# Kernel tuning notes

Measured on AMD Instinct MI355X. Metric: run time of the kernel, lower is better.

## Reference

```python
import jax, jax.numpy as jnp
import numpy as np
import math

B, H, L = 8, 256, 4096
C = 1            # channels
D_STATE = 64
DD = D_STATE // 2  # d = 32
DT_MIN, DT_MAX = 1e-3, 1e-1


def setup_inputs() -> dict:
    key = jax.random.key(0)
    ks = jax.random.split(key, 6)
    u = jax.random.normal(ks[0], (B, H, L), dtype=jnp.float32)
    # analytic init matching the torch module
    h_scale = jnp.exp(jnp.arange(H, dtype=jnp.float32) / H * math.log(DT_MAX / DT_MIN))  # (H,)
    angles = jnp.arange(DD, dtype=jnp.float32) * jnp.float32(np.pi)                      # (DD,)
    theta = jnp.einsum('c,h,d->chd', jnp.ones((C,), jnp.float32), h_scale, angles)       # (C,H,DD)
    a = -jnp.broadcast_to(h_scale[None, :, None], (C, H, DD)).astype(jnp.float32)        # (C,H,DD)
    D = jax.random.normal(ks[1], (C, H), dtype=jnp.float32)
    b_p = jax.random.normal(ks[2], (C, H, DD), dtype=jnp.float32)
    c_p = jax.random.normal(ks[3], (C, H, DD), dtype=jnp.float32)
    x0 = jax.random.normal(ks[4], (C, H, DD), dtype=jnp.float32)
    return {"u": u, "theta": theta, "a": a, "D": D, "b_p": b_p, "c_p": c_p, "x0": x0}


def fft_conv(u, f):
    # u: (B,H,L), f: (C,H,L) -> (B,C,H,L) causal conv via zero-padded FFT
    l = u.shape[-1]
    n = 2 * l
    u_f = jnp.fft.rfft(u, n=n)          # (B,H,n//2+1)
    f_f = jnp.fft.rfft(f, n=n)          # (C,H,n//2+1)
    y_f = jnp.einsum('bhl,chl->bchl', u_f, f_f)
    return jnp.fft.irfft(y_f, n=n)[..., :l]


def reference(u, theta, a, D, b_p, c_p, x0):
    l = u.shape[-1]
    T = 1.0 / (l - 1)
    zk = T * jnp.arange(l, dtype=jnp.float32)            # (L,)
    zk4 = zk[None, None, :, None]                         # (1,1,L,1)
    ls = -jnp.abs(a) + 1j * theta                         # (C,H,DD) complex
    term_0 = (jnp.exp(ls * T) - 1.0) / ls                 # (C,H,DD)
    # base_term: (C,H,L,DD)
    base_term = (2.0 * term_0[:, :, None, :] * jnp.exp(ls[:, :, None, :] * zk4)).real
    q = b_p * c_p                                         # (C,H,DD)
    f = jnp.einsum('chd,chld->chl', q, base_term)         # (C,H,L)
    y = fft_conv(u, f)                                    # (B,C,H,L)
    y = y + jnp.einsum('bhl,ch->bchl', u, D)
    # initial-condition term
    cos_term = 2.0 * T * jnp.exp(-jnp.abs(a)[:, :, None, :] * zk4) * jnp.cos(theta[:, :, None, :] * zk4)
    init = jnp.einsum('chd,chld->chl', 2.0 * (c_p * x0), cos_term)  # (C,H,L)
    y = y + init[None]                                    # broadcast over batch
    b = y.shape[0]
    return y.reshape(b, -1, l)                            # (B, C*H, L)
```

## Files before the change

### kernel.cpp

```cpp
#include <hip/hip_runtime.h>

#define BB 8
#define HH 256
#define LL 4096
#define STR 72

#define WS_H  0
#define WS_P  (2u*1024*1024)
#define WS_R  (4u*1024*1024)
#define WS_C1 (6u*1024*1024)
#define WS_C2 (6u*1024*1024 + 128u*1024)

typedef __attribute__((ext_vector_type(8))) short short8;
typedef __attribute__((ext_vector_type(4))) float f32x4;

static __device__ inline unsigned short f2bf(float x) {
    union { float f; unsigned u; } v; v.f = x;
    unsigned r = v.u + 0x7fffu + ((v.u >> 16) & 1u);
    return (unsigned short)(r >> 16);
}
static __device__ inline float bf2f(unsigned short us) {
    union { unsigned u; float f; } v; v.u = ((unsigned)us) << 16; return v.f;
}

#define CMUL(or_, oi_, ar_, ai_, br_, bi_) do { \
    float _tr = fmaf((ar_), (br_), -(ai_) * (bi_)); \
    float _ti = fmaf((ar_), (bi_), (ai_) * (br_)); \
    (or_) = _tr; (oi_) = _ti; } while (0)

__global__ __launch_bounds__(256) void s4_pre_kernel(
    const float* __restrict__ theta, const float* __restrict__ a,
    const float* __restrict__ b_p,   const float* __restrict__ c_p,
    const float* __restrict__ x0,
    unsigned short* __restrict__ Hm, unsigned short* __restrict__ Pm,
    unsigned short* __restrict__ Rm, float4* __restrict__ C1,
    float* __restrict__ C2)
{
    const int tid = threadIdx.x;
    const int h   = blockIdx.x;
    const int d   = tid & 31;
    const int kb  = tid >> 5;
    const float T = 1.0f / (LL - 1);
    __shared__ float h_s[64];

    const float lr = a[h * 32 + d];
    const float li = theta[h * 32 + d];
    float sn, cS;
    sincosf(li * T, &sn, &cS);
    const float er = expf(lr * T);
    const float Rr = er * cS, Ri = er * sn;
    const float den = lr * lr + li * li;
    const float t0r = ((Rr - 1.f) * lr + Ri * li) / den;
    const float t0i = (Ri * lr - (Rr - 1.f) * li) / den;
    const float qq  = b_p[h * 32 + d] * c_p[h * 32 + d];
    const float wre = 2.f * qq * t0r, wim = 2.f * qq * t0i;
    const float vv  = 4.f * T * c_p[h * 32 + d] * x0[h * 32 + d];

    float r2r, r2i, r4r, r4i, r8r, r8i, r16r, r16i, r32r, r32i;
    CMUL(r2r, r2i, Rr, Ri, Rr, Ri);
    CMUL(r4r, r4i, r2r, r2i, r2r, r2i);
    CMUL(r8r, r8i, r4r, r4i, r4r, r4i);
    CMUL(r16r, r16i, r8r, r8i, r8r, r8i);
    CMUL(r32r, r32i, r16r, r16i, r16r, r16i);

    unsigned short* HmB = Hm + h * 4096;
    unsigned short* PmB = Pm + h * 4096;
    unsigned short* RmB = Rm + h * 4096;

    {
        float pr = 1.f, pi = 0.f;
        if (kb & 1) CMUL(pr, pi, pr, pi, r8r, r8i);
        if (kb & 2) CMUL(pr, pi, pr, pi, r16r, r16i);
        if (kb & 4) CMUL(pr, pi, pr, pi, r32r, r32i);
        #pragma unroll
        for (int k8 = 0; k8 < 8; ++k8) {
            const int k = (kb << 3) + k8;
            RmB[k * 64 + d]           = f2bf(pr);
            RmB[k * 64 + 32 + d]      = f2bf(-pi);
            PmB[d * 64 + (63 - k)]        = f2bf(pr);
            PmB[(32 + d) * 64 + (63 - k)] = f2bf(pi);
            float hk = fmaf(wre, pr, -wim * pi);
            hk += __shfl_xor(hk, 1);
            hk += __shfl_xor(hk, 2);
            hk += __shfl_xor(hk, 4);
            hk += __shfl_xor(hk, 8);
            hk += __shfl_xor(hk, 16);
            if (d == 0) h_s[k] = hk;
            CMUL(pr, pi, pr, pi, Rr, Ri);
        }
    }
    if (tid < 32) {
        float Ar, Ai, wrr, wri;
        CMUL(Ar, Ai, r32r, r32i, r32r, r32i);
        CMUL(wrr, wri, wre, wim, Rr, Ri);
        C1[h * 32 + d] = make_float4(Ar, Ai, wrr, wri);
        C2[h * 32 + d] = vv;
    }
    __syncthreads();

    {
        const int t  = tid >> 2;
        const int tb = (tid & 3) << 4;
        #pragma unroll
        for (int g = 0; g < 4; ++g) {
            const int tau0 = tb + (g << 2);
            unsigned short e[4];
            #pragma unroll
            for (int i = 0; i < 4; ++i) {
                const int dt = t - (tau0 + i);
                e[i] = (dt >= 0) ? f2bf(h_s[dt]) : (unsigned short)0;
            }
            uint2 pk;
            pk.x = (unsigned)e[0] | ((unsigned)e[1] << 16);
            pk.y = (unsigned)e[2] | ((unsigned)e[3] << 16);
            *(uint2*)&HmB[t * 64 + tau0] = pk;
        }
    }
}

__global__ __launch_bounds__(256, 4) void s4_main_kernel(
    const float* __restrict__ u, const float* __restrict__ Dp,
    const unsigned short* __restrict__ Hm, const unsigned short* __restrict__ Pm,
    const unsigned short* __restrict__ Rm, const float4* __restrict__ C1,
    const float* __restrict__ C2, float* __restrict__ out)
{
    const int tid = threadIdx.x;
    const int blk = blockIdx.x;
    const int hh  = blk >> 2;
    const int bp  = blk & 3;

    __shared__ __align__(16) short UsA[64 * STR];
    __shared__ __align__(16) short UsB[64 * STR];
    __shared__ __align__(16) short EQ[64 * STR];
    __shared__ __align__(16) float Seg[32 * 18];

    const int d    = tid & 31;
    const int g    = tid >> 5;
    const int ln   = tid & 63;
    const int m0   = (tid >> 6) << 4;
    const int rowi = ln & 15;
    const int quad = ln >> 4;

    const unsigned short* HmB = Hm + hh * 4096;
    const unsigned short* PmB = Pm + hh * 4096;
    const unsigned short* RmB = Rm + hh * 4096;
    short8 aH[2], aP[2], aR[2];
    #pragma unroll
    for (int kh = 0; kh < 2; ++kh) {
        const int off = (m0 + rowi) * 64 + (kh << 5) + (quad << 3);
        aH[kh] = *(const short8*)&HmB[off];
        aP[kh] = *(const short8*)&PmB[off];
        aR[kh] = *(const short8*)&RmB[off];
    }

    const float* up0 = u + ((((size_t)(bp * 2) * HH) + hh) << 12);
    const float* up1 = u + ((((size_t)(bp * 2 + 1) * HH) + hh) << 12);
    #pragma unroll
    for (int jj = 0; jj < 4; ++jj) {
        const int v  = tid + (jj << 8);
        const float4 val = ((const float4*)up0)[v];
        const int c  = v >> 4;
        const int t0 = (v & 15) << 2;
        uint2 pk;
        pk.x = (unsigned)f2bf(val.x) | ((unsigned)f2bf(val.y) << 16);
        pk.y = (unsigned)f2bf(val.z) | ((unsigned)f2bf(val.w) << 16);
        *(uint2*)&UsA[c * STR + t0] = pk;
    }
    float4 v1[4];
    #pragma unroll
    for (int jj = 0; jj < 4; ++jj)
        v1[jj] = ((const float4*)up1)[tid + (jj << 8)];

    const float4 c1 = C1[hh * 32 + d];
    const float vv  = C2[hh * 32 + d];
    const float Dh  = Dp[hh];
    const float Ar = c1.x, Ai = c1.y;
    float S8r, S8i, S16r, S16i, S32r, S32i;
    {
        float b1r, b1i, b2r, b2i;
        CMUL(b1r, b1i, Ar, Ai, Ar, Ai);
        CMUL(b2r, b2i, b1r, b1i, b1r, b1i);
        CMUL(S8r, S8i, b2r, b2i, b2r, b2i);
        CMUL(S16r, S16i, S8r, S8i, S8r, S8i);
        CMUL(S32r, S32i, S16r, S16i, S16r, S16i);
    }
    __syncthreads();

    #pragma unroll
    for (int it = 0; it < 2; ++it) {
        short* Us = it ? UsB : UsA;

        f32x4 accY[4], accE[4];
        #pragma unroll
        for (int nt = 0; nt < 4; ++nt) {
            accY[nt] = (f32x4){0.f, 0.f, 0.f, 0.f};
            accE[nt] = (f32x4){0.f, 0.f, 0.f, 0.f};
        }
        #pragma unroll
        for (int kh = 0; kh < 2; ++kh) {
            const int k0 = kh << 5;
            #pragma unroll
            for (int nt = 0; nt < 4; ++nt) {
                const short8 bU = *(const short8*)&Us[((nt << 4) + rowi) * STR + k0 + (quad << 3)];
                accY[nt] = __builtin_amdgcn_mfma_f32_16x16x32_bf16(aH[kh], bU, accY[nt], 0, 0, 0);
                accE[nt] = __builtin_amdgcn_mfma_f32_16x16x32_bf16(aP[kh], bU, accE[nt], 0, 0, 0);
            }
        }

        #pragma unroll
        for (int nt = 0; nt < 4; ++nt) {
            uint2 pk;
            pk.x = (unsigned)f2bf(accE[nt][0]) | ((unsigned)f2bf(accE[nt][1]) << 16);
            pk.y = (unsigned)f2bf(accE[nt][2]) | ((unsigned)f2bf(accE[nt][3]) << 16);
            *(uint2*)&EQ[((nt << 4) + rowi) * STR + m0 + (quad << 2)] = pk;
        }

        if (it == 0) {
            #pragma unroll
            for (int jj = 0; jj < 4; ++jj) {
                const int v  = tid + (jj << 8);
                const int c  = v >> 4;
                const int t0 = (v & 15) << 2;
                uint2 pk;
                pk.x = (unsigned)f2bf(v1[jj].x) | ((unsigned)f2bf(v1[jj].y) << 16);
                pk.y = (unsigned)f2bf(v1[jj].z) | ((unsigned)f2bf(v1[jj].w) << 16);
                *(uint2*)&UsB[c * STR + t0] = pk;
            }
        }
        __syncthreads();

        const int cb = g << 3;
        float Er[8], Ei[8];
        {
            float Sr = 0.f, Si = 0.f;
            #pragma unroll
            for (int i = 0; i < 8; ++i) {
                const int c = cb + i;
                Er[i] = bf2f((unsigned short)EQ[c * STR + d]);
                Ei[i] = bf2f((unsigned short)EQ[c * STR + 32 + d]);
                const float nr = fmaf(Ar, Sr, fmaf(-Ai, Si, Er[i]));
                const float ni = fmaf(Ar, Si, fmaf(Ai, Sr, Ei[i]));
                Sr = nr; Si = ni;
            }
            Seg[d * 18 + (g << 1)]     = Sr;
            Seg[d * 18 + (g << 1) + 1] = Si;
        }
        __syncthreads();

        {
            float offr = 0.f, offi = 0.f;
            #pragma unroll
            for (int gp = 0; gp < 7; ++gp) {
                const float2 sg = *(const float2*)&Seg[d * 18 + (gp << 1)];
                const float nr = fmaf(S8r, offr, fmaf(-S8i, offi, sg.x));
                const float ni = fmaf(S8r, offi, fmaf(S8i, offr, sg.y));
                const bool take = gp < g;
                offr = take ? nr : offr;
                offi = take ? ni : offi;
            }
            float Gr = vv, Gi = 0.f;
            if (g & 1) { float nr, ni; CMUL(nr, ni, Gr, Gi, S8r, S8i);   Gr = nr; Gi = ni; }
            if (g & 2) { float nr, ni; CMUL(nr, ni, Gr, Gi, S16r, S16i); Gr = nr; Gi = ni; }
            if (g & 4) { float nr, ni; CMUL(nr, ni, Gr, Gi, S32r, S32i); Gr = nr; Gi = ni; }
            const float wrr = c1.z, wri = c1.w;
            float Sr = offr, Si = offi;
            #pragma unroll
            for (int i = 0; i < 8; ++i) {
                const int c = cb + i;
                const float Qr = fmaf(wrr, Sr, fmaf(-wri, Si, Gr));
                const float Qi = fmaf(wrr, Si, fmaf(wri, Sr, Gi));
                EQ[c * STR + d]      = (short)f2bf(Qr);
                EQ[c * STR + 32 + d] = (short)f2bf(Qi);
                const float nr = fmaf(Ar, Sr, fmaf(-Ai, Si, Er[i]));
                const float ni = fmaf(Ar, Si, fmaf(Ai, Sr, Ei[i]));
                Sr = nr; Si = ni;
                float nGr, nGi;
                CMUL(nGr, nGi, Ar, Ai, Gr, Gi);
                Gr = nGr; Gi = nGi;
            }
        }
        __syncthreads();

        #pragma unroll
        for (int kh = 0; kh < 2; ++kh) {
            const int k0 = kh << 5;
            #pragma unroll
            for (int nt = 0; nt < 4; ++nt) {
                const short8 bQ = *(const short8*)&EQ[((nt << 4) + rowi) * STR + k0 + (quad << 3)];
                accY[nt] = __builtin_amdgcn_mfma_f32_16x16x32_bf16(aR[kh], bQ, accY[nt], 0, 0, 0);
            }
        }

        float* op = out + ((((size_t)(bp * 2 + it) * HH) + hh) << 12);
        #pragma unroll
        for (int nt = 0; nt < 4; ++nt) {
            const int c    = (nt << 4) + rowi;
            const int toff = m0 + (quad << 2);
            const uint2 uu = *(const uint2*)&Us[c * STR + toff];
            float4 res;
            res.x = fmaf(Dh, bf2f((unsigned short)(uu.x & 0xffffu)), accY[nt][0]);
            res.y = fmaf(Dh, bf2f((unsigned short)(uu.x >> 16)),     accY[nt][1]);
            res.z = fmaf(Dh, bf2f((unsigned short)(uu.y & 0xffffu)), accY[nt][2]);
            res.w = fmaf(Dh, bf2f((unsigned short)(uu.y >> 16)),     accY[nt][3]);
            *(float4*)&op[c * 64 + toff] = res;
        }
        __syncthreads();
    }
}

extern "C" void kernel_launch(void* const* d_in, const int* in_sizes, int n_in,
                              void* d_out, int out_size, void* d_ws, size_t ws_size,
                              hipStream_t stream) {
    const float* u     = (const float*)d_in[0];
    const float* theta = (const float*)d_in[1];
    const float* a     = (const float*)d_in[2];
    const float* Dp    = (const float*)d_in[3];
    const float* b_p   = (const float*)d_in[4];
    const float* c_p   = (const float*)d_in[5];
    const float* x0    = (const float*)d_in[6];
    float* out = (float*)d_out;
    char* ws = (char*)d_ws;
    unsigned short* Hm = (unsigned short*)(ws + WS_H);
    unsigned short* Pm = (unsigned short*)(ws + WS_P);
    unsigned short* Rm = (unsigned short*)(ws + WS_R);
    float4*         C1 = (float4*)(ws + WS_C1);
    float*          C2 = (float*)(ws + WS_C2);

    hipLaunchKernelGGL(s4_pre_kernel, dim3(HH), dim3(256), 0, stream,
                       theta, a, b_p, c_p, x0, Hm, Pm, Rm, C1, C2);
    hipLaunchKernelGGL(s4_main_kernel, dim3(HH * 4), dim3(256), 0, stream,
                       u, Dp, Hm, Pm, Rm, C1, C2, out);
}
```

Before: 104.7 us.

## Fuse filter precompute into main kernel, building matrices in shared memory

```diff
diff --git a/kernel.cpp b/kernel.cpp
--- a/kernel.cpp
+++ b/kernel.cpp
@@ -5,12 +5,6 @@
 #define LL 4096
 #define STR 72
 
-#define WS_H  0
-#define WS_P  (2u*1024*1024)
-#define WS_R  (4u*1024*1024)
-#define WS_C1 (6u*1024*1024)
-#define WS_C2 (6u*1024*1024 + 128u*1024)
-
 typedef __attribute__((ext_vector_type(8))) short short8;
 typedef __attribute__((ext_vector_type(4))) float f32x4;
 
@@ -28,23 +22,41 @@
     float _ti = fmaf((ar_), (bi_), (ai_) * (br_)); \
     (or_) = _tr; (oi_) = _ti; } while (0)
 
-__global__ __launch_bounds__(256) void s4_pre_kernel(
-    const float* __restrict__ theta, const float* __restrict__ a,
-    const float* __restrict__ b_p,   const float* __restrict__ c_p,
-    const float* __restrict__ x0,
-    unsigned short* __restrict__ Hm, unsigned short* __restrict__ Pm,
-    unsigned short* __restrict__ Rm, float4* __restrict__ C1,
-    float* __restrict__ C2)
+__global__ __launch_bounds__(256, 4) void s4_fused_kernel(
+    const float* __restrict__ u, const float* __restrict__ theta,
+    const float* __restrict__ a, const float* __restrict__ Dp,
+    const float* __restrict__ b_p, const float* __restrict__ c_p,
+    const float* __restrict__ x0, float* __restrict__ out)
 {
     const int tid = threadIdx.x;
-    const int h   = blockIdx.x;
-    const int d   = tid & 31;
-    const int kb  = tid >> 5;
+    const int blk = blockIdx.x;
+    const int hh  = blk >> 2;
+    const int bp  = blk & 3;
+
+    __shared__ __align__(16) short UsA[64 * STR];
+    __shared__ __align__(16) short UsB[64 * STR];
+    __shared__ __align__(16) short EQ[64 * STR];
+    __shared__ __align__(16) float Seg[32 * 18];
+    __shared__ float h_s[64];
+
+    const int d    = tid & 31;
+    const int kb   = tid >> 5;
+    const int g    = tid >> 5;
+    const int ln   = tid & 63;
+    const int m0   = (tid >> 6) << 4;
+    const int rowi = ln & 15;
+    const int quad = ln >> 4;
+
+    const float* up0 = u + ((((size_t)(bp * 2) * HH) + hh) << 12);
+    const float* up1 = u + ((((size_t)(bp * 2 + 1) * HH) + hh) << 12);
+    float4 v0[4];
+    #pragma unroll
+    for (int jj = 0; jj < 4; ++jj)
+        v0[jj] = ((const float4*)up0)[tid + (jj << 8)];
+
     const float T = 1.0f / (LL - 1);
-    __shared__ float h_s[64];
-
-    const float lr = a[h * 32 + d];
-    const float li = theta[h * 32 + d];
+    const float lr = a[hh * 32 + d];
+    const float li = theta[hh * 32 + d];
     float sn, cS;
     sincosf(li * T, &sn, &cS);
     const float er = expf(lr * T);
@@ -52,9 +64,10 @@
     const float den = lr * lr + li * li;
     const float t0r = ((Rr - 1.f) * lr + Ri * li) / den;
     const float t0i = (Ri * lr - (Rr - 1.f) * li) / den;
-    const float qq  = b_p[h * 32 + d] * c_p[h * 32 + d];
+    const float qq  = b_p[hh * 32 + d] * c_p[hh * 32 + d];
     const float wre = 2.f * qq * t0r, wim = 2.f * qq * t0i;
-    const float vv  = 4.f * T * c_p[h * 32 + d] * x0[h * 32 + d];
+    const float vv  = 4.f * T * c_p[hh * 32 + d] * x0[hh * 32 + d];
+    const float Dh  = Dp[hh];
 
     float r2r, r2i, r4r, r4i, r8r, r8i, r16r, r16i, r32r, r32i;
     CMUL(r2r, r2i, Rr, Ri, Rr, Ri);
@@ -63,10 +76,6 @@
     CMUL(r16r, r16i, r8r, r8i, r8r, r8i);
     CMUL(r32r, r32i, r16r, r16i, r16r, r16i);
 
-    unsigned short* HmB = Hm + h * 4096;
-    unsigned short* PmB = Pm + h * 4096;
-    unsigned short* RmB = Rm + h * 4096;
-
     {
         float pr = 1.f, pi = 0.f;
         if (kb & 1) CMUL(pr, pi, pr, pi, r8r, r8i);
@@ -75,10 +84,10 @@
         #pragma unroll
         for (int k8 = 0; k8 < 8; ++k8) {
             const int k = (kb << 3) + k8;
-            RmB[k * 64 + d]           = f2bf(pr);
-            RmB[k * 64 + 32 + d]      = f2bf(-pi);
-            PmB[d * 64 + (63 - k)]        = f2bf(pr);
-            PmB[(32 + d) * 64 + (63 - k)] = f2bf(pi);
+            EQ[k * STR + d]            = (short)f2bf(pr);
+            EQ[k * STR + 32 + d]       = (short)f2bf(-pi);
+            UsB[d * STR + (63 - k)]        = (short)f2bf(pr);
+            UsB[(32 + d) * STR + (63 - k)] = (short)f2bf(pi);
             float hk = fmaf(wre, pr, -wim * pi);
             hk += __shfl_xor(hk, 1);
             hk += __shfl_xor(hk, 2);
@@ -89,92 +98,10 @@
             CMUL(pr, pi, pr, pi, Rr, Ri);
         }
     }
-    if (tid < 32) {
-        float Ar, Ai, wrr, wri;
-        CMUL(Ar, Ai, r32r, r32i, r32r, r32i);
-        CMUL(wrr, wri, wre, wim, Rr, Ri);
-        C1[h * 32 + d] = make_float4(Ar, Ai, wrr, wri);
-        C2[h * 32 + d] = vv;
-    }
-    __syncthreads();
-
-    {
-        const int t  = tid >> 2;
-        const int tb = (tid & 3) << 4;
-        #pragma unroll
-        for (int g = 0; g < 4; ++g) {
-            const int tau0 = tb + (g << 2);
-            unsigned short e[4];
-            #pragma unroll
-            for (int i = 0; i < 4; ++i) {
-                const int dt = t - (tau0 + i);
-                e[i] = (dt >= 0) ? f2bf(h_s[dt]) : (unsigned short)0;
-            }
-            uint2 pk;
-            pk.x = (unsigned)e[0] | ((unsigned)e[1] << 16);
-            pk.y = (unsigned)e[2] | ((unsigned)e[3] << 16);
-            *(uint2*)&HmB[t * 64 + tau0] = pk;
-        }
-    }
-}
-
-__global__ __launch_bounds__(256, 4) void s4_main_kernel(
-    const float* __restrict__ u, const float* __restrict__ Dp,
-    const unsigned short* __restrict__ Hm, const unsigned short* __restrict__ Pm,
-    const unsigned short* __restrict__ Rm, const float4* __restrict__ C1,
-    const float* __restrict__ C2, float* __restrict__ out)
-{
-    const int tid = threadIdx.x;
-    const int blk = blockIdx.x;
-    const int hh  = blk >> 2;
-    const int bp  = blk & 3;
-
-    __shared__ __align__(16) short UsA[64 * STR];
-    __shared__ __align__(16) short UsB[64 * STR];
-    __shared__ __align__(16) short EQ[64 * STR];
-    __shared__ __align__(16) float Seg[32 * 18];
-
-    const int d    = tid & 31;
-    const int g    = tid >> 5;
-    const int ln   = tid & 63;
-    const int m0   = (tid >> 6) << 4;
-    const int rowi = ln & 15;
-    const int quad = ln >> 4;
-
-    const unsigned short* HmB = Hm + hh * 4096;
-    const unsigned short* PmB = Pm + hh * 4096;
-    const unsigned short* RmB = Rm + hh * 4096;
-    short8 aH[2], aP[2], aR[2];
-    #pragma unroll
-    for (int kh = 0; kh < 2; ++kh) {
-        const int off = (m0 + rowi) * 64 + (kh << 5) + (quad << 3);
-        aH[kh] = *(const short8*)&HmB[off];
-        aP[kh] = *(const short8*)&PmB[off];
-        aR[kh] = *(const short8*)&RmB[off];
-    }
-
-    const float* up0 = u + ((((size_t)(bp * 2) * HH) + hh) << 12);
-    const float* up1 = u + ((((size_t)(bp * 2 + 1) * HH) + hh) << 12);
-    #pragma unroll
-    for (int jj = 0; jj < 4; ++jj) {
-        const int v  = tid + (jj << 8);
-        const float4 val = ((const float4*)up0)[v];
-        const int c  = v >> 4;
-        const int t0 = (v & 15) << 2;
-        uint2 pk;
-        pk.x = (unsigned)f2bf(val.x) | ((unsigned)f2bf(val.y) << 16);
-        pk.y = (unsigned)f2bf(val.z) | ((unsigned)f2bf(val.w) << 16);
-        *(uint2*)&UsA[c * STR + t0] = pk;
-    }
-    float4 v1[4];
-    #pragma unroll
-    for (int jj = 0; jj < 4; ++jj)
-        v1[jj] = ((const float4*)up1)[tid + (jj << 8)];
-
-    const float4 c1 = C1[hh * 32 + d];
-    const float vv  = C2[hh * 32 + d];
-    const float Dh  = Dp[hh];
-    const float Ar = c1.x, Ai = c1.y;
+
+    float Ar, Ai, wrr, wri;
+    CMUL(Ar, Ai, r32r, r32i, r32r, r32i);
+    CMUL(wrr, wri, wre, wim, Rr, Ri);
     float S8r, S8i, S16r, S16i, S32r, S32i;
     {
         float b1r, b1i, b2r, b2i;
@@ -186,6 +113,52 @@
     }
     __syncthreads();
 
+    {
+        const int t  = tid >> 2;
+        const int tb = (tid & 3) << 4;
+        #pragma unroll
+        for (int gg = 0; gg < 4; ++gg) {
+            const int tau0 = tb + (gg << 2);
+            unsigned short e[4];
+            #pragma unroll
+            for (int i = 0; i < 4; ++i) {
+                const int dt = t - (tau0 + i);
+                e[i] = (dt >= 0) ? f2bf(h_s[dt]) : (unsigned short)0;
+            }
+            uint2 pk;
+            pk.x = (unsigned)e[0] | ((unsigned)e[1] << 16);
+            pk.y = (unsigned)e[2] | ((unsigned)e[3] << 16);
+            *(uint2*)&UsA[t * STR + tau0] = pk;
+        }
+    }
+    __syncthreads();
+
+    short8 aH[2], aP[2], aR[2];
+    #pragma unroll
+    for (int kh = 0; kh < 2; ++kh) {
+        const int off = (m0 + rowi) * STR + (kh << 5) + (quad << 3);
+        aH[kh] = *(const short8*)&UsA[off];
+        aP[kh] = *(const short8*)&UsB[off];
+        aR[kh] = *(const short8*)&EQ[off];
+    }
+    __syncthreads();
+
+    #pragma unroll
+    for (int jj = 0; jj < 4; ++jj) {
+        const int v  = tid + (jj << 8);
+        const int c  = v >> 4;
+        const int t0 = (v & 15) << 2;
+        uint2 pk;
+        pk.x = (unsigned)f2bf(v0[jj].x) | ((unsigned)f2bf(v0[jj].y) << 16);
+        pk.y = (unsigned)f2bf(v0[jj].z) | ((unsigned)f2bf(v0[jj].w) << 16);
+        *(uint2*)&UsA[c * STR + t0] = pk;
+    }
+    float4 v1[4];
+    #pragma unroll
+    for (int jj = 0; jj < 4; ++jj)
+        v1[jj] = ((const float4*)up1)[tid + (jj << 8)];
+    __syncthreads();
+
     #pragma unroll
     for (int it = 0; it < 2; ++it) {
         short* Us = it ? UsB : UsA;
@@ -262,7 +235,6 @@
             if (g & 1) { float nr, ni; CMUL(nr, ni, Gr, Gi, S8r, S8i);   Gr = nr; Gi = ni; }
             if (g & 2) { float nr, ni; CMUL(nr, ni, Gr, Gi, S16r, S16i); Gr = nr; Gi = ni; }
             if (g & 4) { float nr, ni; CMUL(nr, ni, Gr, Gi, S32r, S32i); Gr = nr; Gi = ni; }
-            const float wrr = c1.z, wri = c1.w;
             float Sr = offr, Si = offi;
             #pragma unroll
             for (int i = 0; i < 8; ++i) {
@@ -319,15 +291,8 @@
     const float* c_p   = (const float*)d_in[5];
     const float* x0    = (const float*)d_in[6];
     float* out = (float*)d_out;
-    char* ws = (char*)d_ws;
-    unsigned short* Hm = (unsigned short*)(ws + WS_H);
-    unsigned short* Pm = (unsigned short*)(ws + WS_P);
-    unsigned short* Rm = (unsigned short*)(ws + WS_R);
-    float4*         C1 = (float4*)(ws + WS_C1);
-    float*          C2 = (float*)(ws + WS_C2);
-
-    hipLaunchKernelGGL(s4_pre_kernel, dim3(HH), dim3(256), 0, stream,
-                       theta, a, b_p, c_p, x0, Hm, Pm, Rm, C1, C2);
-    hipLaunchKernelGGL(s4_main_kernel, dim3(HH * 4), dim3(256), 0, stream,
-                       u, Dp, Hm, Pm, Rm, C1, C2, out);
-}
+    (void)d_ws; (void)ws_size;
+
+    hipLaunchKernelGGL(s4_fused_kernel, dim3(HH * 4), dim3(256), 0, stream,
+                       u, theta, a, Dp, b_p, c_p, x0, out);
+}
```

Result: faster. 101.7 us (-2.8%).
